# Performance work log

Hardware: AMD Instinct MI355X
Metric: run time of the kernel (lower is better)

The kernel has to match this reference:

```python
import jax, jax.numpy as jnp
import numpy as np

N, D, K = 262144, 64, 1024


def setup_inputs() -> dict:
    key = jax.random.key(0)
    kx, kc = jax.random.split(key)
    x = jax.random.normal(kx, (N, D), dtype=jnp.float32)
    codebook = jax.random.normal(kc, (K, D), dtype=jnp.float32)
    return {"x": x, "codebook": codebook}


def reference(x, codebook):
    # VQTokenizer.encode: cdist(x, codebook) -> argmin -> gather.
    # squared distances equals argmin over cdist (sqrt is monotone).
    x2 = jnp.sum(x * x, axis=-1, keepdims=True)            # (N, 1)
    c2 = jnp.sum(codebook * codebook, axis=-1)             # (K,)
    d2 = x2 + c2[None, :] - 2.0 * jnp.einsum('nd,kd->nk', x, codebook)  # (N, K)
    encoded = jnp.argmin(d2, axis=1)                       # (N,) int
    quantized = jnp.take(codebook, encoded, axis=0)        # (N, D)
    return encoded, quantized
```

## Files before the change

kernel.cpp:

```cpp
#include <hip/hip_runtime.h>
#include <hip/hip_bf16.h>

#define NPTS 262144
#define DDIM 64
#define KCB  1024
#define CHUNK 128
#define NCHUNK (KCB / CHUNK)
#define GPC (CHUNK / 16)
#define PPB 256

typedef __attribute__((ext_vector_type(8))) short short8;
typedef __attribute__((ext_vector_type(4))) float f32x4;

static __device__ __forceinline__ unsigned short f2bf_rne(float f) {
    union { float f; unsigned u; } v; v.f = f;
    unsigned r = v.u + 0x7FFFu + ((v.u >> 16) & 1u);
    return (unsigned short)(r >> 16);
}
static __device__ __forceinline__ float bf2f(unsigned short h) {
    union { unsigned u; float f; } v; v.u = ((unsigned)h) << 16;
    return v.f;
}
static __device__ __forceinline__ bool beats(float sa, int ka, float sb, int kb) {
    return (sa > sb) || (sa == sb && ka < kb);
}
static __device__ __forceinline__ float keyf(float acc, unsigned inv) {
    return __uint_as_float((__float_as_uint(acc) & 0xFFFFFFC0u) | inv);
}

__global__ __launch_bounds__(256) void c2n_kernel(const float* __restrict__ cb,
                                                  float* __restrict__ c2n) {
    int k = blockIdx.x * blockDim.x + threadIdx.x;
    if (k >= KCB) return;
    const float4* row = (const float4*)(cb + (size_t)k * DDIM);
    float s0 = 0.f, s1 = 0.f, s2 = 0.f, s3 = 0.f;
#pragma unroll
    for (int j = 0; j < DDIM / 4; ++j) {
        float4 a = row[j];
        s0 = __builtin_fmaf(a.x, a.x, s0);
        s1 = __builtin_fmaf(a.y, a.y, s1);
        s2 = __builtin_fmaf(a.z, a.z, s2);
        s3 = __builtin_fmaf(a.w, a.w, s3);
    }
    c2n[k] = 256.0f - 0.5f * ((s0 + s1) + (s2 + s3));
}

__global__ __launch_bounds__(256) void pack_kernel(const float* __restrict__ cb,
                                                   unsigned short* __restrict__ G) {
    int t = blockIdx.x * 256 + threadIdx.x;
    int r = t >> 3, d8 = t & 7;
    const float4* src = (const float4*)(cb + (size_t)r * DDIM + d8 * 8);
    float4 v0 = src[0], v1 = src[1];
    float vv[8] = {v0.x, v0.y, v0.z, v0.w, v1.x, v1.y, v1.z, v1.w};
    short8 h, l;
#pragma unroll
    for (int j = 0; j < 8; ++j) {
        unsigned short hb = f2bf_rne(vv[j]);
        h[j] = (short)hb;
        l[j] = (short)f2bf_rne(vv[j] - bf2f(hb));
    }
    int c = r >> 7, g = (r >> 4) & 7, col = r & 15;
    int ks = d8 >> 2, q = d8 & 3;
    size_t base = (size_t)c * 16384 + g * 1024 + ks * 512 + q * 128 + col * 8;
    *(short8*)(G + base) = h;
    *(short8*)(G + base + 8192) = l;
}

struct BFrag { short8 h0, l0, h1, l1; };

__global__ __launch_bounds__(512, 4) void vq_main(const float* __restrict__ x,
                                                  const float* __restrict__ cb,
                                                  const float* __restrict__ c2n,
                                                  const unsigned short* __restrict__ G,
                                                  float* __restrict__ out) {
    __shared__ unsigned short frag[2][CHUNK * DDIM * 2];
    __shared__ float lds_c2f[KCB];
    __shared__ int lds_bk1[PPB];
    __shared__ int lds_bk2[PPB];

    const int tid = threadIdx.x;
    const int lane = tid & 63;
    const int wave = tid >> 6;
    const int b15 = lane & 15;
    const int q = lane >> 4;
    const int blk_base = blockIdx.x * PPB;
    const int wave_base = blk_base + wave * 32;
    const int lane_off = lane * 16;

    short8 Ahi[2][2], Alo[2][2];
#pragma unroll
    for (int t = 0; t < 2; ++t) {
        const float* xr = x + (size_t)(wave_base + t * 16 + b15) * DDIM + q * 8;
#pragma unroll
        for (int ks = 0; ks < 2; ++ks) {
            float4 v0 = *(const float4*)(xr + ks * 32);
            float4 v1 = *(const float4*)(xr + ks * 32 + 4);
            float vv[8] = {v0.x, v0.y, v0.z, v0.w, v1.x, v1.y, v1.z, v1.w};
            short8 h, l;
#pragma unroll
            for (int j = 0; j < 8; ++j) {
                unsigned short hb = f2bf_rne(vv[j]);
                h[j] = (short)hb;
                l[j] = (short)f2bf_rne(vv[j] - bf2f(hb));
            }
            Ahi[t][ks] = h;
            Alo[t][ks] = l;
        }
    }

    float b1[8], b2[8];
#pragma unroll
    for (int i = 0; i < 8; ++i) { b1[i] = 0.0f; b2[i] = 0.0f; }

#define STAGE(cc, buf)                                                                     \
    {                                                                                      \
        const unsigned char* gsrc = (const unsigned char*)G + (size_t)(cc) * 32768 + tid * 16; \
        unsigned char* ldst = (unsigned char*)&frag[buf][0] + tid * 16;                    \
        _Pragma("unroll") for (int it = 0; it < 4; ++it)                                   \
            __builtin_amdgcn_global_load_lds(                                              \
                (const __attribute__((address_space(1))) unsigned int*)(gsrc + it * 8192), \
                (__attribute__((address_space(3))) unsigned int*)(ldst + it * 8192),       \
                16, 0, 0);                                                                 \
    }
#define LOADB(dst, fb, g)                                               \
    {                                                                   \
        const unsigned char* p_ = (fb) + (size_t)(g) * 2048 + lane_off; \
        (dst).h0 = *(const short8*)(p_);                                \
        (dst).l0 = *(const short8*)(p_ + 16384);                        \
        (dst).h1 = *(const short8*)(p_ + 1024);                         \
        (dst).l1 = *(const short8*)(p_ + 17408);                        \
    }
#define COMPUTE(acc, B, cvec)                                                                    \
    {                                                                                            \
        __builtin_amdgcn_s_setprio(1);                                                           \
        _Pragma("unroll") for (int t = 0; t < 2; ++t) {                                          \
            acc[t] = __builtin_amdgcn_mfma_f32_16x16x32_bf16(Ahi[t][0], (B).h0, cvec, 0, 0, 0);  \
            acc[t] = __builtin_amdgcn_mfma_f32_16x16x32_bf16(Ahi[t][0], (B).l0, acc[t], 0, 0, 0);\
            acc[t] = __builtin_amdgcn_mfma_f32_16x16x32_bf16(Alo[t][0], (B).h0, acc[t], 0, 0, 0);\
            acc[t] = __builtin_amdgcn_mfma_f32_16x16x32_bf16(Ahi[t][1], (B).h1, acc[t], 0, 0, 0);\
            acc[t] = __builtin_amdgcn_mfma_f32_16x16x32_bf16(Ahi[t][1], (B).l1, acc[t], 0, 0, 0);\
            acc[t] = __builtin_amdgcn_mfma_f32_16x16x32_bf16(Alo[t][1], (B).h1, acc[t], 0, 0, 0);\
        }                                                                                        \
        __builtin_amdgcn_s_setprio(0);                                                           \
    }

    STAGE(0, 0);
    lds_c2f[tid] = c2n[tid];
    lds_c2f[tid + 512] = c2n[tid + 512];
    __syncthreads();

    for (int c = 0; c < NCHUNK; ++c) {
        const int cur = c & 1;
        if (c + 1 < NCHUNK) STAGE(c + 1, cur ^ 1);
        const unsigned char* fb = (const unsigned char*)&frag[cur][0];

#pragma unroll
        for (int gp = 0; gp < 4; ++gp) {
            const int g0 = gp * 2, g1 = g0 + 1;
            const unsigned inv0 = 63u - (unsigned)(c * GPC + g0);
            BFrag Ba, Bb;
            LOADB(Ba, fb, g0);
            LOADB(Bb, fb, g1);
            const float cg0 = lds_c2f[(c * GPC + g0) * 16 + b15];
            const float cg1 = lds_c2f[(c * GPC + g1) * 16 + b15];

            f32x4 acc0[2];
            const f32x4 cvec0 = (f32x4){cg0, cg0, cg0, cg0};
            COMPUTE(acc0, Ba, cvec0);
            f32x4 acc1[2];
            const f32x4 cvec1 = (f32x4){cg1, cg1, cg1, cg1};
            COMPUTE(acc1, Bb, cvec1);

#pragma unroll
            for (int t = 0; t < 2; ++t)
#pragma unroll
                for (int r = 0; r < 4; ++r) {
                    const int i = t * 4 + r;
                    const float ka = keyf(acc0[t][r], inv0);
                    const float kb = keyf(acc1[t][r], inv0 - 1u);
                    const float med = __builtin_amdgcn_fmed3f(b1[i], ka, kb);
                    float nb1;
                    asm("v_max3_f32 %0, %1, %2, %3"
                        : "=v"(nb1) : "v"(b1[i]), "v"(ka), "v"(kb));
                    b1[i] = nb1;
                    b2[i] = fmaxf(b2[i], med);
                }
        }
        __syncthreads();
    }
#undef STAGE
#undef LOADB
#undef COMPUTE

    unsigned int K1[8], K2[8];
    int I1[8], I2[8];
#pragma unroll
    for (int i = 0; i < 8; ++i) {
        K1[i] = __float_as_uint(b1[i]); I1[i] = (int)(63u - (K1[i] & 63u)) * 16 + b15;
        K2[i] = __float_as_uint(b2[i]); I2[i] = (int)(63u - (K2[i] & 63u)) * 16 + b15;
    }
#pragma unroll
    for (int m = 1; m < 16; m <<= 1) {
#pragma unroll
        for (int i = 0; i < 8; ++i) {
            unsigned int o1 = __shfl_xor(K1[i], m); int oi1 = __shfl_xor(I1[i], m);
            unsigned int o2 = __shfl_xor(K2[i], m); int oi2 = __shfl_xor(I2[i], m);
            bool ob = (o1 > K1[i]) || (o1 == K1[i] && oi1 < I1[i]);
            unsigned int nk1, nk2; int ni1, ni2;
            if (ob) {
                nk1 = o1; ni1 = oi1;
                bool sb = (K1[i] > o2) || (K1[i] == o2 && I1[i] < oi2);
                nk2 = sb ? K1[i] : o2; ni2 = sb ? I1[i] : oi2;
            } else {
                nk1 = K1[i]; ni1 = I1[i];
                bool sb = (o1 > K2[i]) || (o1 == K2[i] && oi1 < I2[i]);
                nk2 = sb ? o1 : K2[i]; ni2 = sb ? oi1 : I2[i];
            }
            K1[i] = nk1; I1[i] = ni1; K2[i] = nk2; I2[i] = ni2;
        }
    }

    if (b15 == 0) {
#pragma unroll
        for (int t = 0; t < 2; ++t)
#pragma unroll
            for (int r = 0; r < 4; ++r) {
                int pl = wave * 32 + t * 16 + q * 4 + r;
                lds_bk1[pl] = I1[t * 4 + r];
                lds_bk2[pl] = I2[t * 4 + r];
            }
    }
    __syncthreads();

    const int pid = tid >> 1;
    const int p = blk_base + pid;
    const int ksel = (tid & 1) ? lds_bk2[pid] : lds_bk1[pid];
    const float4* xr = (const float4*)(x + (size_t)p * DDIM);
    const float4* cr = (const float4*)(cb + (size_t)ksel * DDIM);
    float da = 0.f, db = 0.f;
#pragma unroll
    for (int j = 0; j < 16; ++j) {
        float4 xv = xr[j];
        float4 u = cr[j];
        da = __builtin_fmaf(xv.x, u.x, da); db = __builtin_fmaf(xv.y, u.y, db);
        da = __builtin_fmaf(xv.z, u.z, da); db = __builtin_fmaf(xv.w, u.w, db);
    }
    float a = (da + db) + c2n[ksel];
    float oa = __shfl_xor(a, 1);
    int ok = __shfl_xor(ksel, 1);
    const bool first = ((tid & 1) == 0);
    float a1 = first ? a : oa; int k1 = first ? ksel : ok;
    float a2 = first ? oa : a; int k2 = first ? ok : ksel;
    int kf = beats(a1, k1, a2, k2) ? k1 : k2;

    if (first) out[p] = (float)kf;
    const float4* cf = (const float4*)(cb + (size_t)kf * DDIM + (tid & 1) * 32);
    float4* qo = (float4*)(out + NPTS + (size_t)p * DDIM + (tid & 1) * 32);
#pragma unroll
    for (int j = 0; j < 8; ++j) qo[j] = cf[j];
}

extern "C" void kernel_launch(void* const* d_in, const int* in_sizes, int n_in,
                              void* d_out, int out_size, void* d_ws, size_t ws_size,
                              hipStream_t stream) {
    const float* x = (const float*)d_in[0];
    const float* cb = (const float*)d_in[1];
    float* c2n = (float*)d_ws;
    unsigned short* G = (unsigned short*)((char*)d_ws + 4096);

    hipLaunchKernelGGL(c2n_kernel, dim3(KCB / 256), dim3(256), 0, stream, cb, c2n);
    hipLaunchKernelGGL(pack_kernel, dim3(KCB * 8 / 256), dim3(256), 0, stream, cb, G);
    hipLaunchKernelGGL(vq_main, dim3(NPTS / PPB), dim3(512), 0, stream,
                       x, cb, c2n, G, (float*)d_out);
}
```

Measured before the change: 138.9 us.

## Switch distance MFMA to 32x32x16 tiles with single-candidate top-2 tracking

Replaces the pair of 16x16x32 bf16 MFMA tiles per codebook group with one 32x32x16 MFMA tile covering 32 points by 32 codes. The codebook fragment packing and the LDS layout change to match, and the index tag packed into the key's low bits shrinks from 6 to 5 bits. Top-2 tracking now takes one candidate per step with fmed3 and max, and the cross-lane reduction now spans 32 lanes with 16 values per lane. The aim is fewer MFMA issues and LDS loads per code. In exchange it holds more accumulator and best-value registers and runs a longer shuffle reduction.

```diff
diff --git a/kernel.cpp b/kernel.cpp
--- a/kernel.cpp
+++ b/kernel.cpp
@@ -6,11 +6,11 @@
 #define KCB  1024
 #define CHUNK 128
 #define NCHUNK (KCB / CHUNK)
-#define GPC (CHUNK / 16)
+#define CBPC 4
 #define PPB 256
 
 typedef __attribute__((ext_vector_type(8))) short short8;
-typedef __attribute__((ext_vector_type(4))) float f32x4;
+typedef __attribute__((ext_vector_type(16))) float f32x16;
 
 static __device__ __forceinline__ unsigned short f2bf_rne(float f) {
     union { float f; unsigned u; } v; v.f = f;
@@ -25,7 +25,7 @@
     return (sa > sb) || (sa == sb && ka < kb);
 }
 static __device__ __forceinline__ float keyf(float acc, unsigned inv) {
-    return __uint_as_float((__float_as_uint(acc) & 0xFFFFFFC0u) | inv);
+    return __uint_as_float((__float_as_uint(acc) & 0xFFFFFFE0u) | inv);
 }
 
 __global__ __launch_bounds__(256) void c2n_kernel(const float* __restrict__ cb,
@@ -59,14 +59,12 @@
         h[j] = (short)hb;
         l[j] = (short)f2bf_rne(vv[j] - bf2f(hb));
     }
-    int c = r >> 7, g = (r >> 4) & 7, col = r & 15;
-    int ks = d8 >> 2, q = d8 & 3;
-    size_t base = (size_t)c * 16384 + g * 1024 + ks * 512 + q * 128 + col * 8;
+    int cbk = r >> 5, col = r & 31;
+    int ks = d8 >> 1, kh = d8 & 1;
+    size_t base = (size_t)cbk * 4096 + ks * 512 + kh * 256 + col * 8;
     *(short8*)(G + base) = h;
-    *(short8*)(G + base + 8192) = l;
-}
-
-struct BFrag { short8 h0, l0, h1, l1; };
+    *(short8*)(G + base + 2048) = l;
+}
 
 __global__ __launch_bounds__(512, 4) void vq_main(const float* __restrict__ x,
                                                   const float* __restrict__ cb,
@@ -81,20 +79,19 @@
     const int tid = threadIdx.x;
     const int lane = tid & 63;
     const int wave = tid >> 6;
-    const int b15 = lane & 15;
-    const int q = lane >> 4;
+    const int col = lane & 31;
+    const int kh = lane >> 5;
     const int blk_base = blockIdx.x * PPB;
     const int wave_base = blk_base + wave * 32;
     const int lane_off = lane * 16;
 
-    short8 Ahi[2][2], Alo[2][2];
-#pragma unroll
-    for (int t = 0; t < 2; ++t) {
-        const float* xr = x + (size_t)(wave_base + t * 16 + b15) * DDIM + q * 8;
-#pragma unroll
-        for (int ks = 0; ks < 2; ++ks) {
-            float4 v0 = *(const float4*)(xr + ks * 32);
-            float4 v1 = *(const float4*)(xr + ks * 32 + 4);
+    short8 Ahi[4], Alo[4];
+    {
+        const float* xr = x + (size_t)(wave_base + col) * DDIM + kh * 8;
+#pragma unroll
+        for (int ks = 0; ks < 4; ++ks) {
+            float4 v0 = *(const float4*)(xr + ks * 16);
+            float4 v1 = *(const float4*)(xr + ks * 16 + 4);
             float vv[8] = {v0.x, v0.y, v0.z, v0.w, v1.x, v1.y, v1.z, v1.w};
             short8 h, l;
 #pragma unroll
@@ -103,14 +100,14 @@
                 h[j] = (short)hb;
                 l[j] = (short)f2bf_rne(vv[j] - bf2f(hb));
             }
-            Ahi[t][ks] = h;
-            Alo[t][ks] = l;
-        }
-    }
-
-    float b1[8], b2[8];
-#pragma unroll
-    for (int i = 0; i < 8; ++i) { b1[i] = 0.0f; b2[i] = 0.0f; }
+            Ahi[ks] = h;
+            Alo[ks] = l;
+        }
+    }
+
+    float b1[16], b2[16];
+#pragma unroll
+    for (int i = 0; i < 16; ++i) { b1[i] = 0.0f; b2[i] = 0.0f; }
 
 #define STAGE(cc, buf)                                                                     \
     {                                                                                      \
@@ -122,27 +119,6 @@
                 (__attribute__((address_space(3))) unsigned int*)(ldst + it * 8192),       \
                 16, 0, 0);                                                                 \
     }
-#define LOADB(dst, fb, g)                                               \
-    {                                                                   \
-        const unsigned char* p_ = (fb) + (size_t)(g) * 2048 + lane_off; \
-        (dst).h0 = *(const short8*)(p_);                                \
-        (dst).l0 = *(const short8*)(p_ + 16384);                        \
-        (dst).h1 = *(const short8*)(p_ + 1024);                         \
-        (dst).l1 = *(const short8*)(p_ + 17408);                        \
-    }
-#define COMPUTE(acc, B, cvec)                                                                    \
-    {                                                                                            \
-        __builtin_amdgcn_s_setprio(1);                                                           \
-        _Pragma("unroll") for (int t = 0; t < 2; ++t) {                                          \
-            acc[t] = __builtin_amdgcn_mfma_f32_16x16x32_bf16(Ahi[t][0], (B).h0, cvec, 0, 0, 0);  \
-            acc[t] = __builtin_amdgcn_mfma_f32_16x16x32_bf16(Ahi[t][0], (B).l0, acc[t], 0, 0, 0);\
-            acc[t] = __builtin_amdgcn_mfma_f32_16x16x32_bf16(Alo[t][0], (B).h0, acc[t], 0, 0, 0);\
-            acc[t] = __builtin_amdgcn_mfma_f32_16x16x32_bf16(Ahi[t][1], (B).h1, acc[t], 0, 0, 0);\
-            acc[t] = __builtin_amdgcn_mfma_f32_16x16x32_bf16(Ahi[t][1], (B).l1, acc[t], 0, 0, 0);\
-            acc[t] = __builtin_amdgcn_mfma_f32_16x16x32_bf16(Alo[t][1], (B).h1, acc[t], 0, 0, 0);\
-        }                                                                                        \
-        __builtin_amdgcn_s_setprio(0);                                                           \
-    }
 
     STAGE(0, 0);
     lds_c2f[tid] = c2n[tid];
@@ -155,54 +131,50 @@
         const unsigned char* fb = (const unsigned char*)&frag[cur][0];
 
 #pragma unroll
-        for (int gp = 0; gp < 4; ++gp) {
-            const int g0 = gp * 2, g1 = g0 + 1;
-            const unsigned inv0 = 63u - (unsigned)(c * GPC + g0);
-            BFrag Ba, Bb;
-            LOADB(Ba, fb, g0);
-            LOADB(Bb, fb, g1);
-            const float cg0 = lds_c2f[(c * GPC + g0) * 16 + b15];
-            const float cg1 = lds_c2f[(c * GPC + g1) * 16 + b15];
-
-            f32x4 acc0[2];
-            const f32x4 cvec0 = (f32x4){cg0, cg0, cg0, cg0};
-            COMPUTE(acc0, Ba, cvec0);
-            f32x4 acc1[2];
-            const f32x4 cvec1 = (f32x4){cg1, cg1, cg1, cg1};
-            COMPUTE(acc1, Bb, cvec1);
-
-#pragma unroll
-            for (int t = 0; t < 2; ++t)
-#pragma unroll
-                for (int r = 0; r < 4; ++r) {
-                    const int i = t * 4 + r;
-                    const float ka = keyf(acc0[t][r], inv0);
-                    const float kb = keyf(acc1[t][r], inv0 - 1u);
-                    const float med = __builtin_amdgcn_fmed3f(b1[i], ka, kb);
-                    float nb1;
-                    asm("v_max3_f32 %0, %1, %2, %3"
-                        : "=v"(nb1) : "v"(b1[i]), "v"(ka), "v"(kb));
-                    b1[i] = nb1;
-                    b2[i] = fmaxf(b2[i], med);
-                }
+        for (int cbl = 0; cbl < CBPC; ++cbl) {
+            const int cbg = c * CBPC + cbl;
+            const unsigned inv = 31u - (unsigned)cbg;
+            const unsigned char* pb = fb + cbl * 8192 + lane_off;
+            const float cg = lds_c2f[cbg * 32 + col];
+            f32x16 cvec;
+#pragma unroll
+            for (int i = 0; i < 16; ++i) cvec[i] = cg;
+
+            f32x16 acc;
+            __builtin_amdgcn_s_setprio(1);
+#pragma unroll
+            for (int ks = 0; ks < 4; ++ks) {
+                const short8 Bh = *(const short8*)(pb + ks * 1024);
+                const short8 Bl = *(const short8*)(pb + 4096 + ks * 1024);
+                acc = __builtin_amdgcn_mfma_f32_32x32x16_bf16(
+                    Ahi[ks], Bh, (ks == 0) ? cvec : acc, 0, 0, 0);
+                acc = __builtin_amdgcn_mfma_f32_32x32x16_bf16(Ahi[ks], Bl, acc, 0, 0, 0);
+                acc = __builtin_amdgcn_mfma_f32_32x32x16_bf16(Alo[ks], Bh, acc, 0, 0, 0);
+            }
+            __builtin_amdgcn_s_setprio(0);
+
+#pragma unroll
+            for (int i = 0; i < 16; ++i) {
+                const float kk = keyf(acc[i], inv);
+                b2[i] = __builtin_amdgcn_fmed3f(kk, b1[i], b2[i]);
+                b1[i] = fmaxf(b1[i], kk);
+            }
         }
         __syncthreads();
     }
 #undef STAGE
-#undef LOADB
-#undef COMPUTE
-
-    unsigned int K1[8], K2[8];
-    int I1[8], I2[8];
-#pragma unroll
-    for (int i = 0; i < 8; ++i) {
-        K1[i] = __float_as_uint(b1[i]); I1[i] = (int)(63u - (K1[i] & 63u)) * 16 + b15;
-        K2[i] = __float_as_uint(b2[i]); I2[i] = (int)(63u - (K2[i] & 63u)) * 16 + b15;
-    }
-#pragma unroll
-    for (int m = 1; m < 16; m <<= 1) {
-#pragma unroll
-        for (int i = 0; i < 8; ++i) {
+
+    unsigned int K1[16], K2[16];
+    int I1[16], I2[16];
+#pragma unroll
+    for (int i = 0; i < 16; ++i) {
+        K1[i] = __float_as_uint(b1[i]); I1[i] = (int)(31u - (K1[i] & 31u)) * 32 + col;
+        K2[i] = __float_as_uint(b2[i]); I2[i] = (int)(31u - (K2[i] & 31u)) * 32 + col;
+    }
+#pragma unroll
+    for (int m = 1; m < 32; m <<= 1) {
+#pragma unroll
+        for (int i = 0; i < 16; ++i) {
             unsigned int o1 = __shfl_xor(K1[i], m); int oi1 = __shfl_xor(I1[i], m);
             unsigned int o2 = __shfl_xor(K2[i], m); int oi2 = __shfl_xor(I2[i], m);
             bool ob = (o1 > K1[i]) || (o1 == K1[i] && oi1 < I1[i]);
@@ -220,15 +192,14 @@
         }
     }
 
-    if (b15 == 0) {
-#pragma unroll
-        for (int t = 0; t < 2; ++t)
-#pragma unroll
-            for (int r = 0; r < 4; ++r) {
-                int pl = wave * 32 + t * 16 + q * 4 + r;
-                lds_bk1[pl] = I1[t * 4 + r];
-                lds_bk2[pl] = I2[t * 4 + r];
-            }
+    if (col == 0) {
+#pragma unroll
+        for (int i = 0; i < 16; ++i) {
+            int row = (i & 3) + 8 * (i >> 2) + 4 * kh;
+            int pl = wave * 32 + row;
+            lds_bk1[pl] = I1[i];
+            lds_bk2[pl] = I2[i];
+        }
     }
     __syncthreads();
 
```

Result: slower. 162.0 us (+16.6%).
